# Optimization experiments

Hardware: AMD Instinct MI355X
Metric: run time of the kernel (lower is better)

Reference implementation:

```python
import jax, jax.numpy as jnp
import numpy as np

IN_C, OUT_C, K, STRIDE, PAD = 64, 128, 3, 1, 1
GRID_SIZE, SPLINE_ORDER = 5, 3
GRID_LO, GRID_HI = -1.0, 1.0
IN_DIM = IN_C * K * K  # groups=1 -> 576


def setup_inputs() -> dict:
    key = jax.random.key(0)
    k0, k1, k2, k3 = jax.random.split(key, 4)
    x = jax.random.normal(k0, (16, IN_C, 48, 48), dtype=jnp.float32)
    base_weight = jax.random.normal(k1, (OUT_C, IN_DIM), dtype=jnp.float32) * 0.05
    spline_weight = jax.random.normal(k2, (OUT_C, IN_DIM, GRID_SIZE + SPLINE_ORDER), dtype=jnp.float32) * 0.05
    spline_scaler = 1.0 + jax.random.normal(k3, (OUT_C, IN_DIM), dtype=jnp.float32) * 0.05
    return {"x": x, "base_weight": base_weight, "spline_weight": spline_weight, "spline_scaler": spline_scaler}


def _grid():
    # uniform extended grid, shape (IN_DIM, GRID_SIZE + 2*SPLINE_ORDER + 1)
    h = (GRID_HI - GRID_LO) / GRID_SIZE
    g = jnp.arange(-SPLINE_ORDER, GRID_SIZE + SPLINE_ORDER + 1, dtype=jnp.float32) * h + GRID_LO
    return jnp.broadcast_to(g, (IN_DIM, g.shape[0]))


def b_splines(x, grid):
    # x: (N, in_dim); grid: (in_dim, G). Cox-de Boor recursion.
    xe = x[..., None]
    bases = ((xe >= grid[:, :-1]) & (xe < grid[:, 1:])).astype(x.dtype)
    for k in range(1, SPLINE_ORDER + 1):
        left = (xe - grid[:, : -(k + 1)]) / (grid[:, k:-1] - grid[:, : -(k + 1)]) * bases[..., :-1]
        right = (grid[:, k + 1:] - xe) / (grid[:, k + 1:] - grid[:, 1:-k]) * bases[..., 1:]
        bases = left + right
    return bases  # (N, in_dim, GRID_SIZE + SPLINE_ORDER)


def reference(x, base_weight, spline_weight, spline_scaler):
    B, C, H, W = x.shape
    # im2col: feature dim ordered (c, kh, kw) with spatial fastest, matching F.unfold
    patches = jax.lax.conv_general_dilated_patches(
        x, (K, K), (STRIDE, STRIDE), [(PAD, PAD), (PAD, PAD)],
        dimension_numbers=("NCHW", "OIHW", "NCHW"))  # (B, IN_DIM, Ho, Wo)
    Ho = (H + 2 * PAD - (K - 1) - 1) // STRIDE + 1
    Wo = (W + 2 * PAD - (K - 1) - 1) // STRIDE + 1
    # faithful to the source: view(B, groups, in_dim, L) then view(-1, in_dim), no transpose
    x_unf = patches.reshape(B, 1, IN_DIM, Ho * Wo).reshape(-1, IN_DIM)  # (B*L, IN_DIM)
    grid = _grid()
    base = jax.nn.silu(x_unf) @ base_weight.T  # (N, OUT_C)
    scaled_sw = spline_weight * spline_scaler[..., None]  # (OUT_C, IN_DIM, Gc)
    spl = b_splines(x_unf, grid).reshape(x_unf.shape[0], -1) @ scaled_sw.reshape(OUT_C, -1).T
    return (base + spl).reshape(B, OUT_C, Ho, Wo)
```

## Files before the change

### kernel.cpp

```cpp
#include <hip/hip_runtime.h>
#include <hip/hip_bf16.h>

#define B_N    16
#define C_IN   64
#define QDIM   576
#define OC     128
#define M_TOT  36864
#define NKT    81
#define PLANE  2512

typedef __attribute__((ext_vector_type(8))) short short8;
typedef __attribute__((ext_vector_type(4))) float floatx4;

__device__ __forceinline__ unsigned short f2bf(float f) {
    union { float f; unsigned u; } v; v.f = f;
    unsigned r = (v.u + 0x7FFFu + ((v.u >> 16) & 1u)) >> 16;
    return (unsigned short)r;
}

__device__ __forceinline__ void compute_phi(float x, float* phi) {
    phi[0] = x * __builtin_amdgcn_rcpf(1.0f + __expf(-x));
    float t[12];
#pragma unroll
    for (int i = 0; i < 12; ++i) t[i] = 0.4f * (float)(i - 3) - 1.0f;
    float bb[11];
#pragma unroll
    for (int j = 0; j < 11; ++j) bb[j] = (x >= t[j] && x < t[j + 1]) ? 1.0f : 0.0f;
#pragma unroll
    for (int j = 0; j < 10; ++j)
        bb[j] = (x - t[j]) * 2.5f * bb[j] + (t[j + 2] - x) * 2.5f * bb[j + 1];
#pragma unroll
    for (int j = 0; j < 9; ++j)
        bb[j] = (x - t[j]) * 1.25f * bb[j] + (t[j + 3] - x) * 1.25f * bb[j + 1];
#pragma unroll
    for (int j = 0; j < 8; ++j)
        bb[j] = (x - t[j]) * (2.5f / 3.0f) * bb[j] + (t[j + 4] - x) * (2.5f / 3.0f) * bb[j + 1];
#pragma unroll
    for (int g = 0; g < 8; ++g) phi[1 + g] = bb[g];
}

__global__ __launch_bounds__(256) void phi_kernel(const float* __restrict__ x,
                                                  unsigned short* __restrict__ Phi) {
    int ch = blockIdx.x * 256 + threadIdx.x;
    int bc = ch / 314;
    int cp = ch - bc * 314;
    int p0 = cp * 8;
    const float* xsrc = x + (size_t)bc * 2304;
    short8 v[9];
#pragma unroll
    for (int e = 0; e < 8; ++e) {
        int p = p0 + e;
        int hh = p / 50;
        int ww = p - hh * 50;
        float xv = (hh >= 1 && hh <= 48 && ww >= 1 && ww <= 48) ? xsrc[(hh - 1) * 48 + (ww - 1)] : 0.0f;
        float phi[9];
        compute_phi(xv, phi);
#pragma unroll
        for (int j = 0; j < 9; ++j) v[j][e] = (short)f2bf(phi[j]);
    }
    unsigned short* pdst = Phi + (size_t)bc * 9 * PLANE + p0;
#pragma unroll
    for (int j = 0; j < 9; ++j) *(short8*)(pdst + (size_t)j * PLANE) = v[j];
}

__global__ __launch_bounds__(256) void pack_kernel(const float* __restrict__ bw,
                                                   const float* __restrict__ sw,
                                                   const float* __restrict__ sc,
                                                   unsigned short* __restrict__ Wp) {
    int gtid = blockIdx.x * 256 + threadIdx.x;
    int oc = gtid / QDIM, q = gtid % QDIM;
    float base = bw[gtid];
    float scal = sc[gtid];
    unsigned char* wp8 = (unsigned char*)Wp;
    int kk = q & 63;
    int inner = (oc >> 4) * 2048 + (kk >> 5) * 1024
              + ((((kk >> 3) & 3) << 4) + (oc & 15)) * 16 + (kk & 7) * 2;
    int ktb = q >> 6;
    *(unsigned short*)(wp8 + (size_t)ktb * 16384 + inner) = f2bf(base);
#pragma unroll
    for (int g = 0; g < 8; ++g) {
        float v = sw[(size_t)gtid * 8 + g] * scal;
        *(unsigned short*)(wp8 + (size_t)((g + 1) * 9 + ktb) * 16384 + inner) = f2bf(v);
    }
}

#define MFMA_BF16 __builtin_amdgcn_mfma_f32_16x16x32_bf16

__global__ __launch_bounds__(256, 3) void gemm_kernel(const unsigned short* __restrict__ Phi,
                                                      const unsigned short* __restrict__ Wp,
                                                      float* __restrict__ out) {
    __shared__ __align__(16) unsigned char lds[24960];
    int bid = blockIdx.x;
    int swzb = (bid & 7) * 96 + (bid >> 3);
    int m0 = swzb * 48;
    int tid = threadIdx.x;
    int lane = tid & 63;
    int wv = tid >> 6;
    int wo = wv & 1, wk = wv >> 1;
    int lo = lane & 15, hi = lane >> 4, l7 = lane & 7;

    int s8 = tid & 7;
    int rA = tid >> 3;
    int sxA = s8 ^ (rA & 7);
    int rB = (tid < 128) ? (32 + (tid >> 3)) : rA;
    int sxB = s8 ^ (rB & 7);

    size_t rowb[2];
    int rows[2] = {rA, rB};
#pragma unroll
    for (int i = 0; i < 2; ++i) {
        int n  = m0 + rows[i];
        int b  = n / 2304;
        int u  = n - b * 2304;
        int du = u >> 2;
        int r  = u & 3;
        int c  = du / 9;
        int tap = du - c * 9;
        int kh = tap / 3, kw = tap - kh * 3;
        rowb[i] = ((size_t)(b * C_IN + c) * 9) * PLANE + (size_t)((r * 12 + kh) * 50 + kw);
    }

    auto stageA = [&](int sel, int kt) {
        int j  = kt / 9;
        int q0 = (kt - j * 9) << 6;
        unsigned char* pb = lds + sel * 6144;
        {
            int qs = q0 + sxA * 8;
            int hq = qs / 48, wq = qs - hq * 48;
            const unsigned short* src = Phi + rowb[0] + (size_t)j * PLANE + (size_t)(hq * 50 + wq);
            __builtin_amdgcn_global_load_lds((const __attribute__((address_space(1))) void*)src,
                                             (__attribute__((address_space(3))) void*)(pb + tid * 16), 16, 0, 0);
        }
        if (tid < 128) {
            int qs = q0 + sxB * 8;
            int hq = qs / 48, wq = qs - hq * 48;
            const unsigned short* src = Phi + rowb[1] + (size_t)j * PLANE + (size_t)(hq * 50 + wq);
            __builtin_amdgcn_global_load_lds((const __attribute__((address_space(1))) void*)src,
                                             (__attribute__((address_space(3))) void*)(pb + 4096 + tid * 16), 16, 0, 0);
        }
    };

    const unsigned char* wsrc = (const unsigned char*)Wp
                              + (size_t)wo * 8192 + (size_t)wk * 1024 + (size_t)lane * 16;

#define LOADW(W0, W1, W2, W3, KT) do {                                      \
        const unsigned char* s_ = wsrc + (size_t)(KT) * 16384;              \
        W0 = *(const short8*)(s_);                                          \
        W1 = *(const short8*)(s_ + 2048);                                   \
        W2 = *(const short8*)(s_ + 4096);                                   \
        W3 = *(const short8*)(s_ + 6144);                                   \
    } while (0)

#define COMPUTE(SEL, W0, W1, W2, W3) do {                                   \
        const unsigned char* pb_ = lds + (SEL) * 6144;                      \
        short8 a0_ = *(const short8*)(pb_ + arow0 + sxr);                   \
        short8 a1_ = *(const short8*)(pb_ + arow1 + sxr);                   \
        short8 a2_ = *(const short8*)(pb_ + arow2 + sxr);                   \
        acc[0][0] = MFMA_BF16(a0_, W0, acc[0][0], 0, 0, 0);                 \
        acc[0][1] = MFMA_BF16(a0_, W1, acc[0][1], 0, 0, 0);                 \
        acc[0][2] = MFMA_BF16(a0_, W2, acc[0][2], 0, 0, 0);                 \
        acc[0][3] = MFMA_BF16(a0_, W3, acc[0][3], 0, 0, 0);                 \
        acc[1][0] = MFMA_BF16(a1_, W0, acc[1][0], 0, 0, 0);                 \
        acc[1][1] = MFMA_BF16(a1_, W1, acc[1][1], 0, 0, 0);                 \
        acc[1][2] = MFMA_BF16(a1_, W2, acc[1][2], 0, 0, 0);                 \
        acc[1][3] = MFMA_BF16(a1_, W3, acc[1][3], 0, 0, 0);                 \
        acc[2][0] = MFMA_BF16(a2_, W0, acc[2][0], 0, 0, 0);                 \
        acc[2][1] = MFMA_BF16(a2_, W1, acc[2][1], 0, 0, 0);                 \
        acc[2][2] = MFMA_BF16(a2_, W2, acc[2][2], 0, 0, 0);                 \
        acc[2][3] = MFMA_BF16(a2_, W3, acc[2][3], 0, 0, 0);                 \
    } while (0)

    floatx4 acc[3][4];
    floatx4 zz = {0.f, 0.f, 0.f, 0.f};
#pragma unroll
    for (int a = 0; a < 3; ++a)
#pragma unroll
        for (int b = 0; b < 4; ++b) acc[a][b] = zz;

    int sxr = ((wk * 4 + hi) ^ l7) << 4;
    int arow0 = (0 * 16 + lo) * 128;
    int arow1 = (1 * 16 + lo) * 128;
    int arow2 = (2 * 16 + lo) * 128;

    short8 u0, u1, u2, u3, v0, v1, v2, v3;
    stageA(0, 0);
    LOADW(u0, u1, u2, u3, 0);
    __syncthreads();
    for (int kt = 0; kt < NKT - 1; kt += 2) {
        stageA(1, kt + 1);
        LOADW(v0, v1, v2, v3, kt + 1);
        COMPUTE(0, u0, u1, u2, u3);
        __syncthreads();
        if (kt + 2 < NKT) {
            stageA(0, kt + 2);
            LOADW(u0, u1, u2, u3, kt + 2);
        }
        COMPUTE(1, v0, v1, v2, v3);
        __syncthreads();
    }
    COMPUTE(0, u0, u1, u2, u3);
    __syncthreads();

    float* red = (float*)lds;
    if (wk == 1) {
#pragma unroll
        for (int fm = 0; fm < 3; ++fm)
#pragma unroll
            for (int fo = 0; fo < 4; ++fo)
#pragma unroll
                for (int r = 0; r < 4; ++r)
                    red[(wo * 48 + fm * 16 + hi * 4 + r) * 65 + fo * 16 + lo] = acc[fm][fo][r];
    }
    __syncthreads();
    if (wk == 0) {
#pragma unroll
        for (int fm = 0; fm < 3; ++fm) {
#pragma unroll
            for (int fo = 0; fo < 4; ++fo) {
                int oc = wo * 64 + fo * 16 + lo;
#pragma unroll
                for (int r = 0; r < 4; ++r) {
                    int nrow = m0 + fm * 16 + hi * 4 + r;
                    out[(size_t)nrow * 128 + oc] =
                        acc[fm][fo][r] + red[(wo * 48 + fm * 16 + hi * 4 + r) * 65 + fo * 16 + lo];
                }
            }
        }
    }
#undef LOADW
#undef COMPUTE
}

extern "C" void kernel_launch(void* const* d_in, const int* in_sizes, int n_in,
                              void* d_out, int out_size, void* d_ws, size_t ws_size,
                              hipStream_t stream) {
    const float* x  = (const float*)d_in[0];
    const float* bw = (const float*)d_in[1];
    const float* sw = (const float*)d_in[2];
    const float* sc = (const float*)d_in[3];
    float* out = (float*)d_out;

    unsigned short* Wp  = (unsigned short*)d_ws;
    unsigned short* Phi = (unsigned short*)((char*)d_ws + 1572864);

    pack_kernel<<<288, 256, 0, stream>>>(bw, sw, sc, Wp);
    phi_kernel<<<1256, 256, 0, stream>>>(x, Phi);
    gemm_kernel<<<M_TOT / 48, 256, 0, stream>>>(Phi, Wp, out);
}
```

Measured before the change: 151.4 us.

## Deepen GEMM pipeline to a 4-slot LDS ring with explicit vmcnt waits

Replaces the two-buffer A staging and double-buffered weight registers with a 4-slot LDS ring, three register sets for weights, and a fully unrolled main loop. Each iteration uses one barrier plus hand-tuned s_waitcnt vmcnt counts instead of two __syncthreads. Loads are issued three tiles ahead of the MFMA work, and s_setprio is raised around the MFMA block. The goal is to hide global-to-LDS load latency and cut barrier stalls. The cost is more registers and LDS, and the hard-coded wait counts are fragile.

Result: no change. 149.9 us (-1.0%).

```diff
diff --git a/kernel.cpp b/kernel.cpp
--- a/kernel.cpp
+++ b/kernel.cpp
@@ -120,10 +120,10 @@
         rowb[i] = ((size_t)(b * C_IN + c) * 9) * PLANE + (size_t)((r * 12 + kh) * 50 + kw);
     }
 
-    auto stageA = [&](int sel, int kt) {
+    auto stageA = [&](int slot, int kt) {
         int j  = kt / 9;
         int q0 = (kt - j * 9) << 6;
-        unsigned char* pb = lds + sel * 6144;
+        unsigned char* pb = lds + slot * 6144;
         {
             int qs = q0 + sxA * 8;
             int hq = qs / 48, wq = qs - hq * 48;
@@ -151,11 +151,12 @@
         W3 = *(const short8*)(s_ + 6144);                                   \
     } while (0)
 
-#define COMPUTE(SEL, W0, W1, W2, W3) do {                                   \
-        const unsigned char* pb_ = lds + (SEL) * 6144;                      \
+#define COMPUTE(SLOT, W0, W1, W2, W3) do {                                  \
+        const unsigned char* pb_ = lds + (SLOT) * 6144;                     \
         short8 a0_ = *(const short8*)(pb_ + arow0 + sxr);                   \
         short8 a1_ = *(const short8*)(pb_ + arow1 + sxr);                   \
         short8 a2_ = *(const short8*)(pb_ + arow2 + sxr);                   \
+        __builtin_amdgcn_s_setprio(1);                                      \
         acc[0][0] = MFMA_BF16(a0_, W0, acc[0][0], 0, 0, 0);                 \
         acc[0][1] = MFMA_BF16(a0_, W1, acc[0][1], 0, 0, 0);                 \
         acc[0][2] = MFMA_BF16(a0_, W2, acc[0][2], 0, 0, 0);                 \
@@ -168,6 +169,20 @@
         acc[2][1] = MFMA_BF16(a2_, W1, acc[2][1], 0, 0, 0);                 \
         acc[2][2] = MFMA_BF16(a2_, W2, acc[2][2], 0, 0, 0);                 \
         acc[2][3] = MFMA_BF16(a2_, W3, acc[2][3], 0, 0, 0);                 \
+        __builtin_amdgcn_s_setprio(0);                                      \
+    } while (0)
+
+#define WAITV(N01, N23) do {                                                \
+        if (wv < 2) asm volatile("s_waitcnt vmcnt(" #N01 ")");              \
+        else        asm volatile("s_waitcnt vmcnt(" #N23 ")");              \
+    } while (0)
+
+#define ITER(KT, WC0,WC1,WC2,WC3, WN0,WN1,WN2,WN3, DOSTAGE, DOLOADW, N01, N23) do { \
+        WAITV(N01, N23);                                                    \
+        __builtin_amdgcn_s_barrier();                                       \
+        if (DOSTAGE) stageA(((KT) + 3) & 3, (KT) + 3);                      \
+        if (DOLOADW) LOADW(WN0, WN1, WN2, WN3, (KT) + 2);                   \
+        COMPUTE((KT) & 3, WC0, WC1, WC2, WC3);                              \
     } while (0)
 
     floatx4 acc[3][4];
@@ -182,23 +197,25 @@
     int arow1 = (1 * 16 + lo) * 128;
     int arow2 = (2 * 16 + lo) * 128;
 
-    short8 u0, u1, u2, u3, v0, v1, v2, v3;
-    stageA(0, 0);
+    short8 u0, u1, u2, u3, v0, v1, v2, v3, t0, t1, t2, t3;
+
+    stageA(0, 0); stageA(1, 1); stageA(2, 2);
     LOADW(u0, u1, u2, u3, 0);
-    __syncthreads();
-    for (int kt = 0; kt < NKT - 1; kt += 2) {
-        stageA(1, kt + 1);
-        LOADW(v0, v1, v2, v3, kt + 1);
-        COMPUTE(0, u0, u1, u2, u3);
-        __syncthreads();
-        if (kt + 2 < NKT) {
-            stageA(0, kt + 2);
-            LOADW(u0, u1, u2, u3, kt + 2);
-        }
-        COMPUTE(1, v0, v1, v2, v3);
-        __syncthreads();
-    }
-    COMPUTE(0, u0, u1, u2, u3);
+    LOADW(v0, v1, v2, v3, 1);
+
+    ITER(0, u0,u1,u2,u3, t0,t1,t2,t3, 1, 1, 0, 0);
+
+    for (int kt = 1; kt <= 73; kt += 3) {
+        ITER(kt,     v0,v1,v2,v3, u0,u1,u2,u3, 1, 1, 6, 5);
+        ITER(kt + 1, t0,t1,t2,t3, v0,v1,v2,v3, 1, 1, 6, 5);
+        ITER(kt + 2, u0,u1,u2,u3, t0,t1,t2,t3, 1, 1, 6, 5);
+    }
+    ITER(76, v0,v1,v2,v3, u0,u1,u2,u3, 1, 1, 6, 5);
+    ITER(77, t0,t1,t2,t3, v0,v1,v2,v3, 1, 1, 6, 5);
+    ITER(78, u0,u1,u2,u3, t0,t1,t2,t3, 0, 1, 6, 5);
+    ITER(79, v0,v1,v2,v3, u0,u1,u2,u3, 0, 0, 4, 4);
+    ITER(80, t0,t1,t2,t3, u0,u1,u2,u3, 0, 0, 0, 0);
+
     __syncthreads();
 
     float* red = (float*)lds;
@@ -229,6 +246,8 @@
     }
 #undef LOADW
 #undef COMPUTE
+#undef WAITV
+#undef ITER
 }
 
 extern "C" void kernel_launch(void* const* d_in, const int* in_sizes, int n_in,
```
